# Optimization experiments

Hardware: AMD Instinct MI355X
Metric: run time of the kernel (lower is better)

The kernel has to match this reference:

```python
import jax, jax.numpy as jnp
import numpy as np

N = 50000      # total nodes after flattening [1,1,N,D]
E = 600000     # random edges (plus N self-loops appended)
D = 128        # in_dim == out_dim
H = 8          # num_heads
DP = D // H    # per-head dim (each_out_dim)
SLOPE = 0.2    # DGL GATv2Conv default negative_slope


def setup_inputs() -> dict:
    key = jax.random.key(0)
    ks = jax.random.split(key, 6)
    x = jax.random.normal(ks[0], (1, 1, N, D), dtype=jnp.float32)
    s = 1.0 / np.sqrt(D).astype(np.float32)
    # GATv2Conv params: separate src/dst linear projections (share_weights=False),
    # with bias, plus a per-head attention vector.
    w_src = jax.random.uniform(ks[1], (D, H * DP), jnp.float32, -s, s)
    b_src = jnp.zeros((H * DP,), jnp.float32)
    w_dst = jax.random.uniform(ks[2], (D, H * DP), jnp.float32, -s, s)
    b_dst = jnp.zeros((H * DP,), jnp.float32)
    attn_w = jax.random.uniform(ks[3], (H, DP), jnp.float32, -s, s)
    self_loop = jnp.arange(N, dtype=jnp.int32)
    src = jnp.concatenate([jax.random.randint(ks[4], (E,), 0, N, dtype=jnp.int32), self_loop])
    dst = jnp.concatenate([jax.random.randint(ks[5], (E,), 0, N, dtype=jnp.int32), self_loop])
    return {"x": x, "w_src": w_src, "b_src": b_src, "w_dst": w_dst,
            "b_dst": b_dst, "attn_w": attn_w, "src": src, "dst": dst}


def reference(x, w_src, b_src, w_dst, b_dst, attn_w, src, dst):
    shape = x.shape
    h = x.reshape(-1, shape[3])                       # (N, D)
    n = h.shape[0]
    fs = (h @ w_src + b_src).reshape(n, H, DP)        # (N, H, Dp) source proj
    fd = (h @ w_dst + b_dst).reshape(n, H, DP)        # (N, H, Dp) dest proj
    # GATv2: e_ij = a^T LeakyReLU(W_s h_i + W_d h_j)
    e = jax.nn.leaky_relu(fs[src] + fd[dst], SLOPE)   # (E, H, Dp)
    logits = jnp.einsum('ehd,hd->eh', e, attn_w)      # (E, H)
    # segment softmax over incoming edges of each destination node
    m = jax.ops.segment_max(logits, dst, num_segments=n)
    m = jnp.where(jnp.isfinite(m), m, 0.0)
    ex = jnp.exp(logits - m[dst])                     # (E, H)
    denom = jax.ops.segment_sum(ex, dst, num_segments=n)
    alpha = ex / denom[dst]                           # (E, H)
    # weighted scatter-add aggregation of source features
    out = jax.ops.segment_sum(alpha[:, :, None] * fs[src], dst, num_segments=n)
    return out.reshape(shape)
```

## Files before the change

kernel.cpp:

```cpp
#include <hip/hip_runtime.h>
#include <hip/hip_bf16.h>

#define HH 8
#define DP 16
#define DD 128
#define SLOPE 0.2f

#define BN 64
__global__ __launch_bounds__(256) void proj_count_kernel(
    const float* __restrict__ x,
    const float* __restrict__ w_src, const float* __restrict__ b_src,
    const float* __restrict__ w_dst, const float* __restrict__ b_dst,
    float* __restrict__ fs, float* __restrict__ fd, int n,
    const int* __restrict__ dst, int* __restrict__ count, int ecount) {
  __shared__ float xs[BN][DD];
  const int tid = threadIdx.x;
  const int c = tid & (DD - 1);
  const int m0 = (tid >> 7) * 32;
  const int block0 = blockIdx.x * BN;

  for (int i = tid; i < BN * DD / 4; i += 256) {
    int m = i >> 5;
    int k = (i & 31) << 2;
    int node = block0 + m;
    float4 v = make_float4(0.f, 0.f, 0.f, 0.f);
    if (node < n) v = *reinterpret_cast<const float4*>(x + (size_t)node * DD + k);
    *reinterpret_cast<float4*>(&xs[m][k]) = v;
  }
  __syncthreads();

  float acc_s[32], acc_d[32];
#pragma unroll
  for (int m = 0; m < 32; ++m) { acc_s[m] = 0.f; acc_d[m] = 0.f; }

  for (int k = 0; k < DD; k += 4) {
    float ws0 = w_src[(k + 0) * DD + c];
    float ws1 = w_src[(k + 1) * DD + c];
    float ws2 = w_src[(k + 2) * DD + c];
    float ws3 = w_src[(k + 3) * DD + c];
    float wd0 = w_dst[(k + 0) * DD + c];
    float wd1 = w_dst[(k + 1) * DD + c];
    float wd2 = w_dst[(k + 2) * DD + c];
    float wd3 = w_dst[(k + 3) * DD + c];
#pragma unroll
    for (int m = 0; m < 32; ++m) {
      float4 xv = *reinterpret_cast<const float4*>(&xs[m0 + m][k]);
      acc_s[m] = fmaf(xv.x, ws0, acc_s[m]);
      acc_s[m] = fmaf(xv.y, ws1, acc_s[m]);
      acc_s[m] = fmaf(xv.z, ws2, acc_s[m]);
      acc_s[m] = fmaf(xv.w, ws3, acc_s[m]);
      acc_d[m] = fmaf(xv.x, wd0, acc_d[m]);
      acc_d[m] = fmaf(xv.y, wd1, acc_d[m]);
      acc_d[m] = fmaf(xv.z, wd2, acc_d[m]);
      acc_d[m] = fmaf(xv.w, wd3, acc_d[m]);
    }
  }

  const float bs = b_src[c];
  const float bd = b_dst[c];
#pragma unroll
  for (int m = 0; m < 32; ++m) {
    int node = block0 + m0 + m;
    if (node < n) {
      fs[(size_t)node * DD + c] = acc_s[m] + bs;
      fd[(size_t)node * DD + c] = acc_d[m] + bd;
    }
  }

  const int stride = gridDim.x * 256;
  for (int e = blockIdx.x * 256 + tid; e < ecount; e += stride)
    atomicAdd(&count[dst[e]], 1);
}

__global__ __launch_bounds__(256) void alloc_kernel(const int* __restrict__ count,
                                                    int* __restrict__ cursor,
                                                    int* __restrict__ total, int n) {
  const int lane = threadIdx.x & 63;
  const int wid = threadIdx.x >> 6;
  const int wave = blockIdx.x * 4 + wid;
  const int i0 = wave * 256;

  int excl[4];
  int carry = 0;
#pragma unroll
  for (int j = 0; j < 4; ++j) {
    int i = i0 + j * 64 + lane;
    int v = (i < n) ? count[i] : 0;
    int incl = v;
#pragma unroll
    for (int off = 1; off < 64; off <<= 1) {
      int t = __shfl_up(incl, (unsigned)off, 64);
      if (lane >= off) incl += t;
    }
    excl[j] = carry + incl - v;
    carry += __shfl(incl, 63, 64);
  }
  int base = 0;
  if (lane == 63) base = atomicAdd(total, carry);
  base = __shfl(base, 63, 64);
#pragma unroll
  for (int j = 0; j < 4; ++j) {
    int i = i0 + j * 64 + lane;
    if (i < n) cursor[i] = base + excl[j];
  }
}

__global__ __launch_bounds__(256) void scatter_kernel(const int* __restrict__ src,
                                                      const int* __restrict__ dst,
                                                      int* __restrict__ cursor,
                                                      int* __restrict__ edge_src, int ecount) {
  int e = blockIdx.x * 256 + threadIdx.x;
  if (e < ecount) {
    int pos = atomicAdd(&cursor[dst[e]], 1);
    edge_src[pos] = src[e];
  }
}

__global__ __launch_bounds__(256) void node_kernel(const float* __restrict__ fs,
                                                   const float* __restrict__ fd,
                                                   const float* __restrict__ attn_w,
                                                   const int* __restrict__ cursor,
                                                   const int* __restrict__ count,
                                                   const int* __restrict__ edge_src,
                                                   float* __restrict__ out, int n) {
  const int wid = threadIdx.x >> 6;
  const int lane = threadIdx.x & 63;
  const int node = blockIdx.x * 4 + wid;
  if (node >= n) return;

  const int d0 = lane * 2;
  const float2 aw = *reinterpret_cast<const float2*>(&attn_w[d0]);
  const float2 fdv = *reinterpret_cast<const float2*>(&fd[(size_t)node * DD + d0]);

  const int e1 = __builtin_amdgcn_readfirstlane(cursor[node]);
  const int e0 = e1 - __builtin_amdgcn_readfirstlane(count[node]);

  float mx[4] = {-1e30f, -1e30f, -1e30f, -1e30f};
  float den[4] = {0.f, 0.f, 0.f, 0.f};
  float2 ac[4] = {{0.f, 0.f}, {0.f, 0.f}, {0.f, 0.f}, {0.f, 0.f}};

  auto logit_of = [&](float2 fsv) -> float {
    float t0 = fsv.x + fdv.x; t0 = (t0 > 0.f) ? t0 : t0 * SLOPE;
    float t1 = fsv.y + fdv.y; t1 = (t1 > 0.f) ? t1 : t1 * SLOPE;
    float p = aw.x * t0 + aw.y * t1;
    p += __shfl_xor(p, 1, 64);
    p += __shfl_xor(p, 2, 64);
    p += __shfl_xor(p, 4, 64);
    return p;
  };
  auto upd = [](float& m, float& dn, float2& a, float logit, float2 fsv) {
    float mn = fmaxf(m, logit);
    float sc = __expf(m - mn);
    float p = __expf(logit - mn);
    dn = dn * sc + p;
    a.x = a.x * sc + p * fsv.x;
    a.y = a.y * sc + p * fsv.y;
    m = mn;
  };
  auto gather = [&](int s) -> float2 {
    return *reinterpret_cast<const float2*>(&fs[(size_t)s * DD + d0]);
  };

  int e = e0;
  const int nfull = (e1 - e0) >> 2;
  if (nfull > 0) {
    int i0 = edge_src[e0], i1 = edge_src[e0 + 1];
    int i2 = edge_src[e0 + 2], i3 = edge_src[e0 + 3];
    float2 f0 = gather(i0), f1 = gather(i1), f2 = gather(i2), f3 = gather(i3);
    int b = (1 < nfull) ? e0 + 4 : e0;
    int j0 = edge_src[b], j1 = edge_src[b + 1];
    int j2 = edge_src[b + 2], j3 = edge_src[b + 3];

    for (int g = 1; g < nfull; ++g) {
      float2 h0 = gather(j0), h1 = gather(j1), h2 = gather(j2), h3 = gather(j3);
      int b2 = (g + 1 < nfull) ? e0 + (g + 1) * 4 : e0;
      int k0 = edge_src[b2], k1 = edge_src[b2 + 1];
      int k2 = edge_src[b2 + 2], k3 = edge_src[b2 + 3];
      float l0 = logit_of(f0), l1 = logit_of(f1);
      float l2 = logit_of(f2), l3 = logit_of(f3);
      upd(mx[0], den[0], ac[0], l0, f0);
      upd(mx[1], den[1], ac[1], l1, f1);
      upd(mx[2], den[2], ac[2], l2, f2);
      upd(mx[3], den[3], ac[3], l3, f3);
      f0 = h0; f1 = h1; f2 = h2; f3 = h3;
      j0 = k0; j1 = k1; j2 = k2; j3 = k3;
    }
    float l0 = logit_of(f0), l1 = logit_of(f1);
    float l2 = logit_of(f2), l3 = logit_of(f3);
    upd(mx[0], den[0], ac[0], l0, f0);
    upd(mx[1], den[1], ac[1], l1, f1);
    upd(mx[2], den[2], ac[2], l2, f2);
    upd(mx[3], den[3], ac[3], l3, f3);
    e = e0 + nfull * 4;
  }
  for (; e < e1; ++e) {
    float2 f0 = gather(edge_src[e]);
    float l0 = logit_of(f0);
    upd(mx[0], den[0], ac[0], l0, f0);
  }

  float M = fmaxf(fmaxf(mx[0], mx[1]), fmaxf(mx[2], mx[3]));
  float denom = 0.f, ax = 0.f, ay = 0.f;
#pragma unroll
  for (int j = 0; j < 4; ++j) {
    float s = __expf(mx[j] - M);
    denom += den[j] * s;
    ax += ac[j].x * s;
    ay += ac[j].y * s;
  }

  float inv = (denom > 0.f) ? 1.f / denom : 0.f;
  *reinterpret_cast<float2*>(&out[(size_t)node * DD + d0]) =
      make_float2(ax * inv, ay * inv);
}

extern "C" void kernel_launch(void* const* d_in, const int* in_sizes, int n_in,
                              void* d_out, int out_size, void* d_ws, size_t ws_size,
                              hipStream_t stream) {
  const float* x      = (const float*)d_in[0];
  const float* w_src  = (const float*)d_in[1];
  const float* b_src  = (const float*)d_in[2];
  const float* w_dst  = (const float*)d_in[3];
  const float* b_dst  = (const float*)d_in[4];
  const float* attn_w = (const float*)d_in[5];
  const int* src = (const int*)d_in[6];
  const int* dst = (const int*)d_in[7];
  float* out = (float*)d_out;

  const int n = in_sizes[0] / DD;
  const int ecount = in_sizes[6];

  size_t off = 0;
  float* fs = (float*)((char*)d_ws + off); off += (size_t)n * DD * sizeof(float);
  float* fd = (float*)((char*)d_ws + off); off += (size_t)n * DD * sizeof(float);
  int* edge_src = (int*)((char*)d_ws + off); off += (size_t)ecount * sizeof(int);
  int* cursor   = (int*)((char*)d_ws + off); off += (size_t)n * sizeof(int);
  int* count    = (int*)((char*)d_ws + off); off += (size_t)n * sizeof(int);
  int* total    = (int*)((char*)d_ws + off); off += sizeof(int);
  (void)ws_size;

  hipMemsetAsync(count, 0, (size_t)(n + 1) * sizeof(int), stream);

  const int proj_blocks = (n + BN - 1) / BN;
  proj_count_kernel<<<proj_blocks, 256, 0, stream>>>(
      x, w_src, b_src, w_dst, b_dst, fs, fd, n, dst, count, ecount);
  alloc_kernel<<<(n + 1023) / 1024, 256, 0, stream>>>(count, cursor, total, n);
  scatter_kernel<<<(ecount + 255) / 256, 256, 0, stream>>>(src, dst, cursor, edge_src, ecount);
  node_kernel<<<(n + 3) / 4, 256, 0, stream>>>(fs, fd, attn_w, cursor, count, edge_src, out, n);
}
```

Measured before the change: 267.0 us.

## Compute src/dst projections with bf16 MFMA using pre-transposed weights

```diff
diff --git a/kernel.cpp b/kernel.cpp
--- a/kernel.cpp
+++ b/kernel.cpp
@@ -6,64 +6,89 @@
 #define DD 128
 #define SLOPE 0.2f
 
+typedef __attribute__((ext_vector_type(8))) short bf16x8;
+typedef __attribute__((ext_vector_type(4))) float f32x4;
+
+__device__ __forceinline__ unsigned short f2bf(float f) {
+  unsigned u = __float_as_uint(f);
+  unsigned r = (u + 0x7FFFu + ((u >> 16) & 1u)) >> 16;
+  return (unsigned short)r;
+}
+
+__global__ __launch_bounds__(256) void wconv_kernel(const float* __restrict__ w_src,
+                                                    const float* __restrict__ w_dst,
+                                                    unsigned short* __restrict__ wt) {
+  int i = blockIdx.x * 256 + threadIdx.x;
+  int cg = i >> 7, k = i & 127;
+  float v = (cg < DD) ? w_src[k * DD + cg] : w_dst[k * DD + (cg - DD)];
+  wt[i] = f2bf(v);
+}
+
 #define BN 64
-__global__ __launch_bounds__(256) void proj_count_kernel(
-    const float* __restrict__ x,
-    const float* __restrict__ w_src, const float* __restrict__ b_src,
-    const float* __restrict__ w_dst, const float* __restrict__ b_dst,
+#define LDK 136
+__global__ __launch_bounds__(256) void proj_mfma_count_kernel(
+    const float* __restrict__ x, const unsigned short* __restrict__ wt,
+    const float* __restrict__ b_src, const float* __restrict__ b_dst,
     float* __restrict__ fs, float* __restrict__ fd, int n,
     const int* __restrict__ dst, int* __restrict__ count, int ecount) {
-  __shared__ float xs[BN][DD];
+  __shared__ __align__(16) unsigned short xs[BN * LDK];
   const int tid = threadIdx.x;
-  const int c = tid & (DD - 1);
-  const int m0 = (tid >> 7) * 32;
   const int block0 = blockIdx.x * BN;
 
-  for (int i = tid; i < BN * DD / 4; i += 256) {
+  for (int i = tid; i < BN * 32; i += 256) {
     int m = i >> 5;
-    int k = (i & 31) << 2;
+    int kq = (i & 31) << 2;
     int node = block0 + m;
     float4 v = make_float4(0.f, 0.f, 0.f, 0.f);
-    if (node < n) v = *reinterpret_cast<const float4*>(x + (size_t)node * DD + k);
-    *reinterpret_cast<float4*>(&xs[m][k]) = v;
+    if (node < n) v = *reinterpret_cast<const float4*>(x + (size_t)node * DD + kq);
+    ushort4 h;
+    h.x = f2bf(v.x); h.y = f2bf(v.y); h.z = f2bf(v.z); h.w = f2bf(v.w);
+    *reinterpret_cast<ushort4*>(&xs[m * LDK + kq]) = h;
   }
   __syncthreads();
 
-  float acc_s[32], acc_d[32];
-#pragma unroll
-  for (int m = 0; m < 32; ++m) { acc_s[m] = 0.f; acc_d[m] = 0.f; }
-
-  for (int k = 0; k < DD; k += 4) {
-    float ws0 = w_src[(k + 0) * DD + c];
-    float ws1 = w_src[(k + 1) * DD + c];
-    float ws2 = w_src[(k + 2) * DD + c];
-    float ws3 = w_src[(k + 3) * DD + c];
-    float wd0 = w_dst[(k + 0) * DD + c];
-    float wd1 = w_dst[(k + 1) * DD + c];
-    float wd2 = w_dst[(k + 2) * DD + c];
-    float wd3 = w_dst[(k + 3) * DD + c];
-#pragma unroll
-    for (int m = 0; m < 32; ++m) {
-      float4 xv = *reinterpret_cast<const float4*>(&xs[m0 + m][k]);
-      acc_s[m] = fmaf(xv.x, ws0, acc_s[m]);
-      acc_s[m] = fmaf(xv.y, ws1, acc_s[m]);
-      acc_s[m] = fmaf(xv.z, ws2, acc_s[m]);
-      acc_s[m] = fmaf(xv.w, ws3, acc_s[m]);
-      acc_d[m] = fmaf(xv.x, wd0, acc_d[m]);
-      acc_d[m] = fmaf(xv.y, wd1, acc_d[m]);
-      acc_d[m] = fmaf(xv.z, wd2, acc_d[m]);
-      acc_d[m] = fmaf(xv.w, wd3, acc_d[m]);
-    }
-  }
-
-  const float bs = b_src[c];
-  const float bd = b_dst[c];
-#pragma unroll
-  for (int m = 0; m < 32; ++m) {
-    int node = block0 + m0 + m;
-    if (node < n) {
-      fs[(size_t)node * DD + c] = acc_s[m] + bs;
-      fd[(size_t)node * DD + c] = acc_d[m] + bd;
+  const int lane = tid & 63;
+  const int wv = tid >> 6;
+  const int n0 = wv * 64;
+  const int fr = lane & 15;
+  const int fq = lane >> 4;
+
+  f32x4 acc[4][4] = {};
+
+#pragma unroll
+  for (int kk = 0; kk < DD; kk += 32) {
+    bf16x8 a[4], b[4];
+#pragma unroll
+    for (int mi = 0; mi < 4; ++mi) {
+      const unsigned short* p = &xs[(mi * 16 + fr) * LDK + kk + fq * 8];
+      a[mi] = *reinterpret_cast<const bf16x8*>(p);
+    }
+#pragma unroll
+    for (int ni = 0; ni < 4; ++ni) {
+      const unsigned short* p = &wt[(size_t)(n0 + ni * 16 + fr) * DD + kk + fq * 8];
+      b[ni] = *reinterpret_cast<const bf16x8*>(p);
+    }
+#pragma unroll
+    for (int mi = 0; mi < 4; ++mi)
+#pragma unroll
+      for (int ni = 0; ni < 4; ++ni)
+        acc[mi][ni] = __builtin_amdgcn_mfma_f32_16x16x32_bf16(a[mi], b[ni], acc[mi][ni], 0, 0, 0);
+  }
+
+#pragma unroll
+  for (int ni = 0; ni < 4; ++ni) {
+    int cg = n0 + ni * 16 + fr;
+    bool issrc = cg < DD;
+    int c = issrc ? cg : cg - DD;
+    float bias = issrc ? b_src[c] : b_dst[c];
+    float* __restrict__ op = issrc ? fs : fd;
+#pragma unroll
+    for (int mi = 0; mi < 4; ++mi) {
+#pragma unroll
+      for (int r = 0; r < 4; ++r) {
+        int m = block0 + mi * 16 + fq * 4 + r;
+        if (m < n) op[(size_t)m * DD + c] = acc[mi][ni][r] + bias;
+      }
     }
   }
 
@@ -237,13 +262,16 @@
   int* cursor   = (int*)((char*)d_ws + off); off += (size_t)n * sizeof(int);
   int* count    = (int*)((char*)d_ws + off); off += (size_t)n * sizeof(int);
   int* total    = (int*)((char*)d_ws + off); off += sizeof(int);
+  off = (off + 15) & ~(size_t)15;
+  unsigned short* wt = (unsigned short*)((char*)d_ws + off); off += 256 * DD * sizeof(unsigned short);
   (void)ws_size;
 
   hipMemsetAsync(count, 0, (size_t)(n + 1) * sizeof(int), stream);
 
+  wconv_kernel<<<(256 * DD) / 256, 256, 0, stream>>>(w_src, w_dst, wt);
   const int proj_blocks = (n + BN - 1) / BN;
-  proj_count_kernel<<<proj_blocks, 256, 0, stream>>>(
-      x, w_src, b_src, w_dst, b_dst, fs, fd, n, dst, count, ecount);
+  proj_mfma_count_kernel<<<proj_blocks, 256, 0, stream>>>(
+      x, wt, b_src, b_dst, fs, fd, n, dst, count, ecount);
   alloc_kernel<<<(n + 1023) / 1024, 256, 0, stream>>>(count, cursor, total, n);
   scatter_kernel<<<(ecount + 255) / 256, 256, 0, stream>>>(src, dst, cursor, edge_src, ecount);
   node_kernel<<<(n + 3) / 4, 256, 0, stream>>>(fs, fd, attn_w, cursor, count, edge_src, out, n);
```

New measurement: 233.5 us. -12.6%, faster.
